# Kernel tuning notes

Hardware: AMD Instinct MI355X
Metric: run time of the kernel (lower is better)

Reference implementation:

```python
import jax, jax.numpy as jnp
import numpy as np

B, S, D = 4, 2048, 1024
E, TOP_K = 8, 2
N_FF = 4096
H = int(2 * N_FF / 3)  # 2730, Expert hidden when ffn_multiplier is None


def setup_inputs() -> dict:
    key = jax.random.key(0)
    ks = jax.random.split(key, 8)
    s = 0.02
    return {
        "x": jax.random.normal(ks[0], (B, S, D), jnp.float32),
        "noise": jax.random.normal(ks[1], (B, S, E), jnp.float32),
        "w_route": jax.random.normal(ks[2], (D, E), jnp.float32) * s,
        "b_route": jnp.zeros((E,), jnp.float32),
        "w_noise": jax.random.normal(ks[3], (D, E), jnp.float32) * s,
        "b_noise": jnp.zeros((E,), jnp.float32),
        "w_proj": jax.random.normal(ks[4], (E, D, 2 * H), jnp.float32) * s,  # SwiGLU proj per expert
        "w_down": jax.random.normal(ks[5], (E, H, D), jnp.float32) * s,
    }


def reference(x, noise, w_route, b_route, w_noise, b_noise, w_proj, w_down):
    b, s, d = x.shape
    e = w_route.shape[1]
    n = b * s
    capacity = int(n * TOP_K / e * 1.0)  # capacity_factor = 1.0

    # --- NoisyTopkRouter (temperature = 1.0) ---
    logits = jnp.einsum("bsd,de->bse", x, w_route) + b_route
    noise_scale = jax.nn.softplus(jnp.einsum("bsd,de->bse", x, w_noise) + b_noise)
    noisy = logits + noise * noise_scale
    top_v, top_i = jax.lax.top_k(noisy, TOP_K)  # [b,s,k]
    # softmax over -inf-filled sparse logits == softmax over the top-k values,
    # scattered back to the expert axis
    probs_k = jax.nn.softmax(top_v, axis=-1)  # [b,s,k]
    routing = jnp.sum(jax.nn.one_hot(top_i, e, dtype=x.dtype) * probs_k[..., None], axis=-2)  # [b,s,e]
    router_prob = routing.mean(axis=(0, 1))
    aux_loss = jnp.sum((router_prob - 1.0 / e) ** 2)

    # --- dispatch ---
    flat_x = x.reshape(n, d)
    flat_gate = routing.reshape(n, e)
    hit = jnp.any(top_i.reshape(n, TOP_K)[:, :, None] == jnp.arange(e)[None, None, :], axis=1)  # [n,e]

    def per_expert(mask_e, gate_e, wp, wd):
        # keep first `capacity` selected tokens, in token order (matches torch nonzero order)
        keep = mask_e & (jnp.cumsum(mask_e) <= capacity)
        sel = jnp.argsort(~keep, stable=True)[:capacity]  # selected token ids first, in order
        valid = keep[sel].astype(flat_x.dtype)
        xin = flat_x[sel]  # [capacity, d]
        x1, x2 = jnp.split(xin @ wp, 2, axis=-1)
        out = (jax.nn.silu(x1) * x2) @ wd  # [capacity, d]
        w = gate_e[sel] * valid
        return sel, out * w[:, None]

    sel, contrib = jax.vmap(per_expert)(hit.T, flat_gate.T, w_proj, w_down)  # [e,cap], [e,cap,d]
    updates = jnp.zeros_like(flat_x).at[sel.reshape(-1)].add(contrib.reshape(-1, d))
    return updates.reshape(b, s, d), aux_loss
```

## Files before the change

kernel.cpp:

```cpp
#include <hip/hip_runtime.h>
#include <cstdint>
#include <cstddef>

#define NTOK 8192
#define DMODEL 1024
#define NEXP 8
#define CAP 2048
#define HFF 2730
#define HFF2 5460
#define KPAD 2752

typedef float f32x4 __attribute__((ext_vector_type(4)));
typedef __attribute__((ext_vector_type(8))) short short8;

__device__ inline unsigned short f2bf(float f) {
  union { float f; unsigned u; } v; v.f = f;
  unsigned u = v.u;
  return (unsigned short)((u + 0x7FFFu + ((u >> 16) & 1u)) >> 16);
}

typedef __attribute__((address_space(1))) const void g_void;
typedef __attribute__((address_space(3))) void l_void;
__device__ __forceinline__ void dma16(const void* g, void* l) {
  __builtin_amdgcn_global_load_lds((g_void*)g, (l_void*)l, 16, 0, 0);
}

__global__ void cast_x_kernel(const float* __restrict__ x, unsigned short* __restrict__ xb) {
  size_t i = ((size_t)blockIdx.x * 256 + threadIdx.x) * 8;
  float4 v0 = *(const float4*)(x + i);
  float4 v1 = *(const float4*)(x + i + 4);
  union { short8 v; unsigned short s[8]; } p;
  p.s[0] = f2bf(v0.x); p.s[1] = f2bf(v0.y); p.s[2] = f2bf(v0.z); p.s[3] = f2bf(v0.w);
  p.s[4] = f2bf(v1.x); p.s[5] = f2bf(v1.y); p.s[6] = f2bf(v1.z); p.s[7] = f2bf(v1.w);
  *(short8*)(xb + i) = p.v;
}

__global__ void router_kernel(const float* __restrict__ x,
                              const float* __restrict__ noise,
                              const float* __restrict__ w_route,
                              const float* __restrict__ b_route,
                              const float* __restrict__ w_noise,
                              const float* __restrict__ b_noise,
                              int* __restrict__ topi,
                              float* __restrict__ gates) {
  const int lane = threadIdx.x & 63;
  const int wave = threadIdx.x >> 6;
  const int tok = blockIdx.x * 4 + wave;
  const float* xr = x + (size_t)tok * DMODEL;

  double aR[8], aN[8];
#pragma unroll
  for (int e = 0; e < 8; e++) { aR[e] = 0.0; aN[e] = 0.0; }

  for (int d = lane; d < DMODEL; d += 64) {
    double xv = (double)xr[d];
    const float* wr = w_route + d * 8;
    const float* wn = w_noise + d * 8;
#pragma unroll
    for (int e = 0; e < 8; e++) {
      aR[e] += xv * (double)wr[e];
      aN[e] += xv * (double)wn[e];
    }
  }
#pragma unroll
  for (int off = 32; off > 0; off >>= 1) {
#pragma unroll
    for (int e = 0; e < 8; e++) {
      aR[e] += __shfl_down(aR[e], (unsigned)off, 64);
      aN[e] += __shfl_down(aN[e], (unsigned)off, 64);
    }
  }
  if (lane == 0) {
    double nv[8];
#pragma unroll
    for (int e = 0; e < 8; e++) {
      double lg = aR[e] + (double)b_route[e];
      double ns = aN[e] + (double)b_noise[e];
      double sp = fmax(ns, 0.0) + log1p(exp(-fabs(ns)));
      nv[e] = lg + (double)noise[(size_t)tok * 8 + e] * sp;
    }
    int i0 = 0;
#pragma unroll
    for (int e = 1; e < 8; e++) if (nv[e] > nv[i0]) i0 = e;
    int i1 = (i0 == 0) ? 1 : 0;
#pragma unroll
    for (int e = 0; e < 8; e++) if (e != i0 && nv[e] > nv[i1]) i1 = e;
    double r = exp(nv[i1] - nv[i0]);
    float g0 = (float)(1.0 / (1.0 + r));
    float g1 = (float)(r / (1.0 + r));
    topi[tok * 2] = i0; topi[tok * 2 + 1] = i1;
    gates[tok * 2] = g0; gates[tok * 2 + 1] = g1;
  }
}

__global__ void aux_kernel(const int* __restrict__ topi,
                           const float* __restrict__ gates,
                           float* __restrict__ out) {
  const int t = threadIdx.x;
  float s[8];
#pragma unroll
  for (int e = 0; e < 8; e++) s[e] = 0.f;
  for (int i = t; i < NTOK; i += 256) {
    int i0 = topi[2 * i], i1 = topi[2 * i + 1];
    float g0 = gates[2 * i], g1 = gates[2 * i + 1];
#pragma unroll
    for (int e = 0; e < 8; e++)
      s[e] += (i0 == e ? g0 : 0.f) + (i1 == e ? g1 : 0.f);
  }
  __shared__ float sh[256][8];
#pragma unroll
  for (int e = 0; e < 8; e++) sh[t][e] = s[e];
  __syncthreads();
  for (int stride = 128; stride > 0; stride >>= 1) {
    if (t < stride) {
#pragma unroll
      for (int e = 0; e < 8; e++) sh[t][e] += sh[t + stride][e];
    }
    __syncthreads();
  }
  if (t == 0) {
    float aux = 0.f;
#pragma unroll
    for (int e = 0; e < 8; e++) {
      float p = sh[0][e] / (float)NTOK - 0.125f;
      aux += p * p;
    }
    out[(size_t)NTOK * DMODEL] = aux;
  }
}

__global__ void dispatch_kernel(const int* __restrict__ topi,
                                const float* __restrict__ gates,
                                int* __restrict__ sel,
                                float* __restrict__ gsel) {
  const int e = blockIdx.x;
  const int t = threadIdx.x;
  const int lane = t & 63;
  const int wave = t >> 6;
  __shared__ int waveSum[4];
  __shared__ int runningS;
  if (t == 0) runningS = 0;
  __syncthreads();

  for (int base = 0; base < NTOK; base += 256) {
    int tok = base + t;
    int i0 = topi[2 * tok], i1 = topi[2 * tok + 1];
    bool hit = (i0 == e) || (i1 == e);
    float g = (i0 == e) ? gates[2 * tok] : gates[2 * tok + 1];
    unsigned long long m = __ballot(hit);
    int prefix = __popcll(m & ((1ull << lane) - 1ull));
    if (lane == 63) waveSum[wave] = prefix + (hit ? 1 : 0);
    __syncthreads();
    int waveOff = 0;
    for (int w = 0; w < wave; w++) waveOff += waveSum[w];
    int pos = runningS + waveOff + prefix;
    if (hit && pos < CAP) { sel[e * CAP + pos] = tok; gsel[e * CAP + pos] = g; }
    __syncthreads();
    if (t == 0) runningS += waveSum[0] + waveSum[1] + waveSum[2] + waveSum[3];
    __syncthreads();
  }
  int total = runningS;
  for (int p = total + t; p < CAP; p += 256) { sel[e * CAP + p] = 0; gsel[e * CAP + p] = 0.f; }
}

__global__ void transpose_wp_kernel(const float* __restrict__ wp,
                                    unsigned short* __restrict__ wpT) {
  const int e = blockIdx.z, d0 = blockIdx.y * 32, f0 = blockIdx.x * 32;
  __shared__ unsigned short tile[32][33];
  const int t = threadIdx.x;
  {
    int ld = t >> 3, lf4 = (t & 7) * 4;
    if (f0 + lf4 < HFF2) {
      float4 v = *(const float4*)(wp + (size_t)e * DMODEL * HFF2 + (size_t)(d0 + ld) * HFF2 + f0 + lf4);
      tile[ld][lf4 + 0] = f2bf(v.x);
      tile[ld][lf4 + 1] = f2bf(v.y);
      tile[ld][lf4 + 2] = f2bf(v.z);
      tile[ld][lf4 + 3] = f2bf(v.w);
    }
  }
  __syncthreads();
  {
    int lf = t >> 3, ldq = (t & 7) * 4;
    if (f0 + lf < HFF2) {
      ushort4 o = make_ushort4(tile[ldq + 0][lf], tile[ldq + 1][lf],
                               tile[ldq + 2][lf], tile[ldq + 3][lf]);
      *(ushort4*)(wpT + (size_t)e * HFF2 * DMODEL + (size_t)(f0 + lf) * DMODEL + d0 + ldq) = o;
    }
  }
}

__global__ void transpose_wd_kernel(const float* __restrict__ wd,
                                    unsigned short* __restrict__ wdT) {
  const int e = blockIdx.z, d0 = blockIdx.y * 32, k0 = blockIdx.x * 32;
  __shared__ unsigned short tile[32][33];
  const int t = threadIdx.x;
  {
    int lk = t >> 3, ld4 = (t & 7) * 4;
    int k = k0 + lk;
    if (k < HFF) {
      float4 v = *(const float4*)(wd + (size_t)e * HFF * DMODEL + (size_t)k * DMODEL + d0 + ld4);
      tile[lk][ld4 + 0] = f2bf(v.x);
      tile[lk][ld4 + 1] = f2bf(v.y);
      tile[lk][ld4 + 2] = f2bf(v.z);
      tile[lk][ld4 + 3] = f2bf(v.w);
    } else {
      tile[lk][ld4 + 0] = 0; tile[lk][ld4 + 1] = 0;
      tile[lk][ld4 + 2] = 0; tile[lk][ld4 + 3] = 0;
    }
  }
  __syncthreads();
  {
    int ld = t >> 3, lkq = (t & 7) * 4;
    ushort4 o = make_ushort4(tile[lkq + 0][ld], tile[lkq + 1][ld],
                             tile[lkq + 2][ld], tile[lkq + 3][ld]);
    *(ushort4*)(wdT + (size_t)e * DMODEL * KPAD + (size_t)(d0 + ld) * KPAD + k0 + lkq) = o;
  }
}

__global__ __launch_bounds__(256, 2)
void gemm1_kernel(const unsigned short* __restrict__ xb,
                  const unsigned short* __restrict__ wpT,
                  const int* __restrict__ sel,
                  unsigned short* __restrict__ h) {
  const int e = blockIdx.z;
  const int m0 = blockIdx.y * 128;
  const int n0 = blockIdx.x * 128;

  __shared__ __align__(16) unsigned short As[128 * 32];
  __shared__ __align__(16) unsigned short B1s[128 * 32];
  __shared__ __align__(16) unsigned short B2s[128 * 32];

  const int t = threadIdx.x;
  const int lane = t & 63;
  const int w = t >> 6;
  const int wm = (w >> 1) * 64;
  const int wn = (w & 1) * 64;
  const int fr = lane & 15;
  const int fq = lane >> 4;

  const int r0 = t >> 2;
  const int seg = (t & 3) * 8;
  const int tok0 = sel[e * CAP + m0 + r0];
  const int tok1 = sel[e * CAP + m0 + 64 + r0];
  const unsigned short* ga0 = xb + (size_t)tok0 * DMODEL + seg;
  const unsigned short* ga1 = xb + (size_t)tok1 * DMODEL + seg;
  const size_t ebase = (size_t)e * HFF2;
  int c0 = n0 + r0;       if (c0 >= HFF) c0 = HFF - 1;
  int c1 = n0 + 64 + r0;  if (c1 >= HFF) c1 = HFF - 1;
  const unsigned short* gb10 = wpT + (ebase + (size_t)c0) * DMODEL + seg;
  const unsigned short* gb11 = wpT + (ebase + (size_t)c1) * DMODEL + seg;
  const unsigned short* gb20 = wpT + (ebase + (size_t)(HFF + c0)) * DMODEL + seg;
  const unsigned short* gb21 = wpT + (ebase + (size_t)(HFF + c1)) * DMODEL + seg;

  unsigned short* aD0 = As + (w * 16) * 32;
  unsigned short* aD1 = As + (64 + w * 16) * 32;
  unsigned short* b1D0 = B1s + (w * 16) * 32;
  unsigned short* b1D1 = B1s + (64 + w * 16) * 32;
  unsigned short* b2D0 = B2s + (w * 16) * 32;
  unsigned short* b2D1 = B2s + (64 + w * 16) * 32;

  f32x4 acc1[4][4], acc2[4][4];
#pragma unroll
  for (int i = 0; i < 4; i++)
#pragma unroll
    for (int j = 0; j < 4; j++) { acc1[i][j] = (f32x4)0.f; acc2[i][j] = (f32x4)0.f; }

  for (int k0 = 0; k0 < DMODEL; k0 += 32) {
    dma16(ga0 + k0, aD0);
    dma16(ga1 + k0, aD1);
    dma16(gb10 + k0, b1D0);
    dma16(gb11 + k0, b1D1);
    dma16(gb20 + k0, b2D0);
    dma16(gb21 + k0, b2D1);
    __syncthreads();

    short8 a[4], b1[4], b2[4];
#pragma unroll
    for (int i = 0; i < 4; i++)
      a[i] = *(const short8*)(As + (wm + i * 16 + fr) * 32 + fq * 8);
#pragma unroll
    for (int j = 0; j < 4; j++) {
      b1[j] = *(const short8*)(B1s + (wn + j * 16 + fr) * 32 + fq * 8);
      b2[j] = *(const short8*)(B2s + (wn + j * 16 + fr) * 32 + fq * 8);
    }
#pragma unroll
    for (int i = 0; i < 4; i++)
#pragma unroll
      for (int j = 0; j < 4; j++) {
        acc1[i][j] = __builtin_amdgcn_mfma_f32_16x16x32_bf16(a[i], b1[j], acc1[i][j], 0, 0, 0);
        acc2[i][j] = __builtin_amdgcn_mfma_f32_16x16x32_bf16(a[i], b2[j], acc2[i][j], 0, 0, 0);
      }
    __syncthreads();
  }

#pragma unroll
  for (int i = 0; i < 4; i++) {
#pragma unroll
    for (int j = 0; j < 4; j++) {
      const int col = n0 + wn + j * 16 + fr;
      if (col < KPAD) {
#pragma unroll
        for (int r = 0; r < 4; r++) {
          const int row = m0 + wm + i * 16 + fq * 4 + r;
          float v1 = acc1[i][j][r], v2 = acc2[i][j][r];
          float hv = (col < HFF) ? (v1 / (1.f + __expf(-v1))) * v2 : 0.f;
          h[((size_t)e * CAP + row) * KPAD + col] = f2bf(hv);
        }
      }
    }
  }
}

__global__ __launch_bounds__(256, 2)
void gemm2_kernel(const unsigned short* __restrict__ h,
                  const unsigned short* __restrict__ wdT,
                  const int* __restrict__ sel,
                  const float* __restrict__ gsel,
                  float* __restrict__ out) {
  const int e = blockIdx.z;
  const int m0 = blockIdx.y * 128;
  const int n0 = blockIdx.x * 128;

  __shared__ __align__(16) unsigned short As[128 * 32];
  __shared__ __align__(16) unsigned short Bs[128 * 32];
  __shared__ int selS[128];
  __shared__ float gS[128];

  const int t = threadIdx.x;
  if (t < 128) { selS[t] = sel[e * CAP + m0 + t]; gS[t] = gsel[e * CAP + m0 + t]; }

  const int lane = t & 63;
  const int w = t >> 6;
  const int wm = (w >> 1) * 64;
  const int wn = (w & 1) * 64;
  const int fr = lane & 15;
  const int fq = lane >> 4;

  const int r0 = t >> 2;
  const int seg = (t & 3) * 8;
  const unsigned short* ga0 = h + ((size_t)e * CAP + m0 + r0) * KPAD + seg;
  const unsigned short* ga1 = h + ((size_t)e * CAP + m0 + 64 + r0) * KPAD + seg;
  const unsigned short* gb0 = wdT + ((size_t)e * DMODEL + n0 + r0) * KPAD + seg;
  const unsigned short* gb1 = wdT + ((size_t)e * DMODEL + n0 + 64 + r0) * KPAD + seg;

  unsigned short* aD0 = As + (w * 16) * 32;
  unsigned short* aD1 = As + (64 + w * 16) * 32;
  unsigned short* bD0 = Bs + (w * 16) * 32;
  unsigned short* bD1 = Bs + (64 + w * 16) * 32;

  f32x4 acc[4][4];
#pragma unroll
  for (int i = 0; i < 4; i++)
#pragma unroll
    for (int j = 0; j < 4; j++) acc[i][j] = (f32x4)0.f;

  for (int k0 = 0; k0 < KPAD; k0 += 32) {
    dma16(ga0 + k0, aD0);
    dma16(ga1 + k0, aD1);
    dma16(gb0 + k0, bD0);
    dma16(gb1 + k0, bD1);
    __syncthreads();

    short8 a[4], b[4];
#pragma unroll
    for (int i = 0; i < 4; i++)
      a[i] = *(const short8*)(As + (wm + i * 16 + fr) * 32 + fq * 8);
#pragma unroll
    for (int j = 0; j < 4; j++)
      b[j] = *(const short8*)(Bs + (wn + j * 16 + fr) * 32 + fq * 8);
#pragma unroll
    for (int i = 0; i < 4; i++)
#pragma unroll
      for (int j = 0; j < 4; j++)
        acc[i][j] = __builtin_amdgcn_mfma_f32_16x16x32_bf16(a[i], b[j], acc[i][j], 0, 0, 0);
    __syncthreads();
  }

#pragma unroll
  for (int i = 0; i < 4; i++) {
#pragma unroll
    for (int j = 0; j < 4; j++) {
      const int col = n0 + wn + j * 16 + fr;
#pragma unroll
      for (int r = 0; r < 4; r++) {
        const int rowL = wm + i * 16 + fq * 4 + r;
        float g = gS[rowL];
        if (g != 0.f) {
          int token = selS[rowL];
          atomicAdd(&out[(size_t)token * DMODEL + col], acc[i][j][r] * g);
        }
      }
    }
  }
}

extern "C" void kernel_launch(void* const* d_in, const int* in_sizes, int n_in,
                              void* d_out, int out_size, void* d_ws, size_t ws_size,
                              hipStream_t stream) {
  const float* x = (const float*)d_in[0];
  const float* noise = (const float*)d_in[1];
  const float* w_route = (const float*)d_in[2];
  const float* b_route = (const float*)d_in[3];
  const float* w_noise = (const float*)d_in[4];
  const float* b_noise = (const float*)d_in[5];
  const float* w_proj = (const float*)d_in[6];
  const float* w_down = (const float*)d_in[7];
  float* out = (float*)d_out;

  char* ws = (char*)d_ws;
  const size_t WT_BYTES = (size_t)NEXP * HFF2 * DMODEL * 2;
  const size_t H_BYTES = (size_t)NEXP * CAP * KPAD * 2;
  unsigned short* wT = (unsigned short*)ws;
  unsigned short* hbuf = (unsigned short*)(ws + WT_BYTES);
  char* p = ws + WT_BYTES + H_BYTES;
  int* sel = (int*)p;          p += (size_t)NEXP * CAP * 4;
  float* gsel = (float*)p;     p += (size_t)NEXP * CAP * 4;
  int* topi = (int*)p;         p += (size_t)NTOK * 2 * 4;
  float* gates = (float*)p;

  unsigned short* xb = (unsigned short*)d_out;

  hipLaunchKernelGGL(cast_x_kernel, dim3(NTOK * DMODEL / (256 * 8)), dim3(256), 0, stream, x, xb);
  hipLaunchKernelGGL(router_kernel, dim3(NTOK / 4), dim3(256), 0, stream,
                     x, noise, w_route, b_route, w_noise, b_noise, topi, gates);
  hipLaunchKernelGGL(dispatch_kernel, dim3(NEXP), dim3(256), 0, stream, topi, gates, sel, gsel);
  hipLaunchKernelGGL(transpose_wp_kernel, dim3(171, 32, NEXP), dim3(256), 0, stream, w_proj, wT);
  hipLaunchKernelGGL(gemm1_kernel, dim3(22, 16, NEXP), dim3(256), 0, stream, xb, wT, sel, hbuf);

  hipMemsetAsync(d_out, 0, (size_t)out_size * sizeof(float), stream);
  hipLaunchKernelGGL(aux_kernel, dim3(1), dim3(256), 0, stream, topi, gates, out);
  hipLaunchKernelGGL(transpose_wd_kernel, dim3(KPAD / 32, DMODEL / 32, NEXP), dim3(256), 0, stream, w_down, wT);
  hipLaunchKernelGGL(gemm2_kernel, dim3(DMODEL / 128, CAP / 128, NEXP), dim3(256), 0, stream,
                     hbuf, wT, sel, gsel, out);
}
```

Measured before the change: 927.1 us.

## Double-buffer swizzled GEMM tiles and replace atomic scatter with gather combine

Result: faster. 850.2 us (-8.3%).

```diff
diff --git a/kernel.cpp b/kernel.cpp
--- a/kernel.cpp
+++ b/kernel.cpp
@@ -17,6 +17,9 @@
   union { float f; unsigned u; } v; v.f = f;
   unsigned u = v.u;
   return (unsigned short)((u + 0x7FFFu + ((u >> 16) & 1u)) >> 16);
+}
+__device__ inline float bf2f(unsigned short s) {
+  union { unsigned u; float f; } v; v.u = ((unsigned)s) << 16; return v.f;
 }
 
 typedef __attribute__((address_space(1))) const void g_void;
@@ -132,35 +135,48 @@
 __global__ void dispatch_kernel(const int* __restrict__ topi,
                                 const float* __restrict__ gates,
                                 int* __restrict__ sel,
-                                float* __restrict__ gsel) {
+                                float* __restrict__ gsel,
+                                int* __restrict__ slot) {
   const int e = blockIdx.x;
   const int t = threadIdx.x;
   const int lane = t & 63;
-  const int wave = t >> 6;
-  __shared__ int waveSum[4];
+  const int w = t >> 6;
+  __shared__ int waveCnt[16];
   __shared__ int runningS;
   if (t == 0) runningS = 0;
   __syncthreads();
 
-  for (int base = 0; base < NTOK; base += 256) {
+  for (int base = 0; base < NTOK; base += 1024) {
     int tok = base + t;
     int i0 = topi[2 * tok], i1 = topi[2 * tok + 1];
     bool hit = (i0 == e) || (i1 == e);
-    float g = (i0 == e) ? gates[2 * tok] : gates[2 * tok + 1];
+    int kth = (i0 == e) ? 0 : 1;
+    float g = gates[2 * tok + kth];
     unsigned long long m = __ballot(hit);
     int prefix = __popcll(m & ((1ull << lane) - 1ull));
-    if (lane == 63) waveSum[wave] = prefix + (hit ? 1 : 0);
-    __syncthreads();
-    int waveOff = 0;
-    for (int w = 0; w < wave; w++) waveOff += waveSum[w];
-    int pos = runningS + waveOff + prefix;
-    if (hit && pos < CAP) { sel[e * CAP + pos] = tok; gsel[e * CAP + pos] = g; }
-    __syncthreads();
-    if (t == 0) runningS += waveSum[0] + waveSum[1] + waveSum[2] + waveSum[3];
-    __syncthreads();
-  }
-  int total = runningS;
-  for (int p = total + t; p < CAP; p += 256) { sel[e * CAP + p] = 0; gsel[e * CAP + p] = 0.f; }
+    if (lane == 63) waveCnt[w] = prefix + (hit ? 1 : 0);
+    __syncthreads();
+    int off = runningS;
+    for (int ww = 0; ww < w; ww++) off += waveCnt[ww];
+    int pos = off + prefix;
+    if (hit) {
+      if (pos < CAP) {
+        sel[e * CAP + pos] = tok; gsel[e * CAP + pos] = g;
+        slot[2 * tok + kth] = pos;
+      } else {
+        slot[2 * tok + kth] = -1;
+      }
+    }
+    __syncthreads();
+    if (t == 0) {
+      int sacc = 0;
+#pragma unroll
+      for (int ww = 0; ww < 16; ww++) sacc += waveCnt[ww];
+      runningS += sacc;
+    }
+    __syncthreads();
+  }
+  for (int p = runningS + t; p < CAP; p += 1024) { sel[e * CAP + p] = 0; gsel[e * CAP + p] = 0.f; }
 }
 
 __global__ void transpose_wp_kernel(const float* __restrict__ wp,
@@ -223,12 +239,12 @@
                   const int* __restrict__ sel,
                   unsigned short* __restrict__ h) {
   const int e = blockIdx.z;
-  const int m0 = blockIdx.y * 128;
-  const int n0 = blockIdx.x * 128;
-
-  __shared__ __align__(16) unsigned short As[128 * 32];
-  __shared__ __align__(16) unsigned short B1s[128 * 32];
-  __shared__ __align__(16) unsigned short B2s[128 * 32];
+  const int m0 = blockIdx.x * 128;
+  const int n0 = blockIdx.y * 128;
+
+  __shared__ __align__(16) unsigned short As[2 * 4096];
+  __shared__ __align__(16) unsigned short B1s[2 * 4096];
+  __shared__ __align__(16) unsigned short B2s[2 * 4096];
 
   const int t = threadIdx.x;
   const int lane = t & 63;
@@ -237,27 +253,23 @@
   const int wn = (w & 1) * 64;
   const int fr = lane & 15;
   const int fq = lane >> 4;
+  const int csw = (fq ^ ((fr >> 1) & 3)) * 8;
 
   const int r0 = t >> 2;
-  const int seg = (t & 3) * 8;
+  const int sw = ((t & 3) ^ ((t >> 3) & 3)) * 8;
   const int tok0 = sel[e * CAP + m0 + r0];
   const int tok1 = sel[e * CAP + m0 + 64 + r0];
-  const unsigned short* ga0 = xb + (size_t)tok0 * DMODEL + seg;
-  const unsigned short* ga1 = xb + (size_t)tok1 * DMODEL + seg;
+  const unsigned short* ga0 = xb + (size_t)tok0 * DMODEL + sw;
+  const unsigned short* ga1 = xb + (size_t)tok1 * DMODEL + sw;
   const size_t ebase = (size_t)e * HFF2;
   int c0 = n0 + r0;       if (c0 >= HFF) c0 = HFF - 1;
   int c1 = n0 + 64 + r0;  if (c1 >= HFF) c1 = HFF - 1;
-  const unsigned short* gb10 = wpT + (ebase + (size_t)c0) * DMODEL + seg;
-  const unsigned short* gb11 = wpT + (ebase + (size_t)c1) * DMODEL + seg;
-  const unsigned short* gb20 = wpT + (ebase + (size_t)(HFF + c0)) * DMODEL + seg;
-  const unsigned short* gb21 = wpT + (ebase + (size_t)(HFF + c1)) * DMODEL + seg;
-
-  unsigned short* aD0 = As + (w * 16) * 32;
-  unsigned short* aD1 = As + (64 + w * 16) * 32;
-  unsigned short* b1D0 = B1s + (w * 16) * 32;
-  unsigned short* b1D1 = B1s + (64 + w * 16) * 32;
-  unsigned short* b2D0 = B2s + (w * 16) * 32;
-  unsigned short* b2D1 = B2s + (64 + w * 16) * 32;
+  const unsigned short* gb10 = wpT + (ebase + (size_t)c0) * DMODEL + sw;
+  const unsigned short* gb11 = wpT + (ebase + (size_t)c1) * DMODEL + sw;
+  const unsigned short* gb20 = wpT + (ebase + (size_t)(HFF + c0)) * DMODEL + sw;
+  const unsigned short* gb21 = wpT + (ebase + (size_t)(HFF + c1)) * DMODEL + sw;
+
+  const int dOff = (w * 16) * 32;
 
   f32x4 acc1[4][4], acc2[4][4];
 #pragma unroll
@@ -265,23 +277,33 @@
 #pragma unroll
     for (int j = 0; j < 4; j++) { acc1[i][j] = (f32x4)0.f; acc2[i][j] = (f32x4)0.f; }
 
+  auto stage = [&](int k0, int buf) {
+    const int bo = buf * 4096;
+    dma16(ga0 + k0, As + bo + dOff);
+    dma16(ga1 + k0, As + bo + 2048 + dOff);
+    dma16(gb10 + k0, B1s + bo + dOff);
+    dma16(gb11 + k0, B1s + bo + 2048 + dOff);
+    dma16(gb20 + k0, B2s + bo + dOff);
+    dma16(gb21 + k0, B2s + bo + 2048 + dOff);
+  };
+
+  stage(0, 0);
   for (int k0 = 0; k0 < DMODEL; k0 += 32) {
-    dma16(ga0 + k0, aD0);
-    dma16(ga1 + k0, aD1);
-    dma16(gb10 + k0, b1D0);
-    dma16(gb11 + k0, b1D1);
-    dma16(gb20 + k0, b2D0);
-    dma16(gb21 + k0, b2D1);
-    __syncthreads();
-
+    const int cur = (k0 >> 5) & 1;
+    __syncthreads();
+    if (k0 + 32 < DMODEL) stage(k0 + 32, cur ^ 1);
+
+    const unsigned short* Ab = As + cur * 4096;
+    const unsigned short* B1b = B1s + cur * 4096;
+    const unsigned short* B2b = B2s + cur * 4096;
     short8 a[4], b1[4], b2[4];
 #pragma unroll
     for (int i = 0; i < 4; i++)
-      a[i] = *(const short8*)(As + (wm + i * 16 + fr) * 32 + fq * 8);
+      a[i] = *(const short8*)(Ab + (wm + i * 16 + fr) * 32 + csw);
 #pragma unroll
     for (int j = 0; j < 4; j++) {
-      b1[j] = *(const short8*)(B1s + (wn + j * 16 + fr) * 32 + fq * 8);
-      b2[j] = *(const short8*)(B2s + (wn + j * 16 + fr) * 32 + fq * 8);
+      b1[j] = *(const short8*)(B1b + (wn + j * 16 + fr) * 32 + csw);
+      b2[j] = *(const short8*)(B2b + (wn + j * 16 + fr) * 32 + csw);
     }
 #pragma unroll
     for (int i = 0; i < 4; i++)
@@ -290,7 +312,6 @@
         acc1[i][j] = __builtin_amdgcn_mfma_f32_16x16x32_bf16(a[i], b1[j], acc1[i][j], 0, 0, 0);
         acc2[i][j] = __builtin_amdgcn_mfma_f32_16x16x32_bf16(a[i], b2[j], acc2[i][j], 0, 0, 0);
       }
-    __syncthreads();
   }
 
 #pragma unroll
@@ -311,42 +332,34 @@
   }
 }
 
-__global__ __launch_bounds__(256, 2)
+__global__ __launch_bounds__(256, 3)
 void gemm2_kernel(const unsigned short* __restrict__ h,
                   const unsigned short* __restrict__ wdT,
-                  const int* __restrict__ sel,
-                  const float* __restrict__ gsel,
-                  float* __restrict__ out) {
+                  unsigned short* __restrict__ contrib) {
   const int e = blockIdx.z;
-  const int m0 = blockIdx.y * 128;
-  const int n0 = blockIdx.x * 128;
-
-  __shared__ __align__(16) unsigned short As[128 * 32];
-  __shared__ __align__(16) unsigned short Bs[128 * 32];
-  __shared__ int selS[128];
-  __shared__ float gS[128];
-
-  const int t = threadIdx.x;
-  if (t < 128) { selS[t] = sel[e * CAP + m0 + t]; gS[t] = gsel[e * CAP + m0 + t]; }
-
+  const int m0 = blockIdx.x * 128;
+  const int n0 = blockIdx.y * 128;
+
+  __shared__ __align__(16) unsigned short As[2 * 4096];
+  __shared__ __align__(16) unsigned short Bs[2 * 4096];
+
+  const int t = threadIdx.x;
   const int lane = t & 63;
   const int w = t >> 6;
   const int wm = (w >> 1) * 64;
   const int wn = (w & 1) * 64;
   const int fr = lane & 15;
   const int fq = lane >> 4;
+  const int csw = (fq ^ ((fr >> 1) & 3)) * 8;
 
   const int r0 = t >> 2;
-  const int seg = (t & 3) * 8;
-  const unsigned short* ga0 = h + ((size_t)e * CAP + m0 + r0) * KPAD + seg;
-  const unsigned short* ga1 = h + ((size_t)e * CAP + m0 + 64 + r0) * KPAD + seg;
-  const unsigned short* gb0 = wdT + ((size_t)e * DMODEL + n0 + r0) * KPAD + seg;
-  const unsigned short* gb1 = wdT + ((size_t)e * DMODEL + n0 + 64 + r0) * KPAD + seg;
-
-  unsigned short* aD0 = As + (w * 16) * 32;
-  unsigned short* aD1 = As + (64 + w * 16) * 32;
-  unsigned short* bD0 = Bs + (w * 16) * 32;
-  unsigned short* bD1 = Bs + (64 + w * 16) * 32;
+  const int sw = ((t & 3) ^ ((t >> 3) & 3)) * 8;
+  const unsigned short* ga0 = h + ((size_t)e * CAP + m0 + r0) * KPAD + sw;
+  const unsigned short* ga1 = h + ((size_t)e * CAP + m0 + 64 + r0) * KPAD + sw;
+  const unsigned short* gb0 = wdT + ((size_t)e * DMODEL + n0 + r0) * KPAD + sw;
+  const unsigned short* gb1 = wdT + ((size_t)e * DMODEL + n0 + 64 + r0) * KPAD + sw;
+
+  const int dOff = (w * 16) * 32;
 
   f32x4 acc[4][4];
 #pragma unroll
@@ -354,26 +367,34 @@
 #pragma unroll
     for (int j = 0; j < 4; j++) acc[i][j] = (f32x4)0.f;
 
+  auto stage = [&](int k0, int buf) {
+    const int bo = buf * 4096;
+    dma16(ga0 + k0, As + bo + dOff);
+    dma16(ga1 + k0, As + bo + 2048 + dOff);
+    dma16(gb0 + k0, Bs + bo + dOff);
+    dma16(gb1 + k0, Bs + bo + 2048 + dOff);
+  };
+
+  stage(0, 0);
   for (int k0 = 0; k0 < KPAD; k0 += 32) {
-    dma16(ga0 + k0, aD0);
-    dma16(ga1 + k0, aD1);
-    dma16(gb0 + k0, bD0);
-    dma16(gb1 + k0, bD1);
-    __syncthreads();
-
+    const int cur = (k0 >> 5) & 1;
+    __syncthreads();
+    if (k0 + 32 < KPAD) stage(k0 + 32, cur ^ 1);
+
+    const unsigned short* Ab = As + cur * 4096;
+    const unsigned short* Bb = Bs + cur * 4096;
     short8 a[4], b[4];
 #pragma unroll
     for (int i = 0; i < 4; i++)
-      a[i] = *(const short8*)(As + (wm + i * 16 + fr) * 32 + fq * 8);
+      a[i] = *(const short8*)(Ab + (wm + i * 16 + fr) * 32 + csw);
 #pragma unroll
     for (int j = 0; j < 4; j++)
-      b[j] = *(const short8*)(Bs + (wn + j * 16 + fr) * 32 + fq * 8);
+      b[j] = *(const short8*)(Bb + (wn + j * 16 + fr) * 32 + csw);
 #pragma unroll
     for (int i = 0; i < 4; i++)
 #pragma unroll
       for (int j = 0; j < 4; j++)
         acc[i][j] = __builtin_amdgcn_mfma_f32_16x16x32_bf16(a[i], b[j], acc[i][j], 0, 0, 0);
-    __syncthreads();
   }
 
 #pragma unroll
@@ -383,15 +404,35 @@
       const int col = n0 + wn + j * 16 + fr;
 #pragma unroll
       for (int r = 0; r < 4; r++) {
-        const int rowL = wm + i * 16 + fq * 4 + r;
-        float g = gS[rowL];
-        if (g != 0.f) {
-          int token = selS[rowL];
-          atomicAdd(&out[(size_t)token * DMODEL + col], acc[i][j][r] * g);
-        }
+        const int row = m0 + wm + i * 16 + fq * 4 + r;
+        contrib[((size_t)e * CAP + row) * DMODEL + col] = f2bf(acc[i][j][r]);
       }
     }
   }
+}
+
+__global__ void combine_kernel(const unsigned short* __restrict__ contrib,
+                               const int* __restrict__ topi,
+                               const int* __restrict__ slot,
+                               const float* __restrict__ gates,
+                               float* __restrict__ out) {
+  const int tok = blockIdx.x;
+  const int t = threadIdx.x;
+  const int e0 = topi[2 * tok], e1 = topi[2 * tok + 1];
+  const int s0 = slot[2 * tok], s1 = slot[2 * tok + 1];
+  const float g0 = gates[2 * tok], g1 = gates[2 * tok + 1];
+  float4 acc = make_float4(0.f, 0.f, 0.f, 0.f);
+  if (s0 >= 0) {
+    ushort4 c = *(const ushort4*)(contrib + ((size_t)(e0 * CAP + s0)) * DMODEL + t * 4);
+    acc.x += g0 * bf2f(c.x); acc.y += g0 * bf2f(c.y);
+    acc.z += g0 * bf2f(c.z); acc.w += g0 * bf2f(c.w);
+  }
+  if (s1 >= 0) {
+    ushort4 c = *(const ushort4*)(contrib + ((size_t)(e1 * CAP + s1)) * DMODEL + t * 4);
+    acc.x += g1 * bf2f(c.x); acc.y += g1 * bf2f(c.y);
+    acc.z += g1 * bf2f(c.z); acc.w += g1 * bf2f(c.w);
+  }
+  *(float4*)(out + (size_t)tok * DMODEL + t * 4) = acc;
 }
 
 extern "C" void kernel_launch(void* const* d_in, const int* in_sizes, int n_in,
@@ -409,27 +450,30 @@
 
   char* ws = (char*)d_ws;
   const size_t WT_BYTES = (size_t)NEXP * HFF2 * DMODEL * 2;
+  const size_t WDT_BYTES = (size_t)NEXP * DMODEL * KPAD * 2;
   const size_t H_BYTES = (size_t)NEXP * CAP * KPAD * 2;
   unsigned short* wT = (unsigned short*)ws;
+  unsigned short* contrib = (unsigned short*)(ws + WDT_BYTES);
   unsigned short* hbuf = (unsigned short*)(ws + WT_BYTES);
   char* p = ws + WT_BYTES + H_BYTES;
   int* sel = (int*)p;          p += (size_t)NEXP * CAP * 4;
   float* gsel = (float*)p;     p += (size_t)NEXP * CAP * 4;
   int* topi = (int*)p;         p += (size_t)NTOK * 2 * 4;
-  float* gates = (float*)p;
+  float* gates = (float*)p;    p += (size_t)NTOK * 2 * 4;
+  int* slot = (int*)p;
 
   unsigned short* xb = (unsigned short*)d_out;
 
   hipLaunchKernelGGL(cast_x_kernel, dim3(NTOK * DMODEL / (256 * 8)), dim3(256), 0, stream, x, xb);
   hipLaunchKernelGGL(router_kernel, dim3(NTOK / 4), dim3(256), 0, stream,
                      x, noise, w_route, b_route, w_noise, b_noise, topi, gates);
-  hipLaunchKernelGGL(dispatch_kernel, dim3(NEXP), dim3(256), 0, stream, topi, gates, sel, gsel);
+  hipLaunchKernelGGL(dispatch_kernel, dim3(NEXP), dim3(1024), 0, stream, topi, gates, sel, gsel, slot);
   hipLaunchKernelGGL(transpose_wp_kernel, dim3(171, 32, NEXP), dim3(256), 0, stream, w_proj, wT);
-  hipLaunchKernelGGL(gemm1_kernel, dim3(22, 16, NEXP), dim3(256), 0, stream, xb, wT, sel, hbuf);
-
-  hipMemsetAsync(d_out, 0, (size_t)out_size * sizeof(float), stream);
+  hipLaunchKernelGGL(gemm1_kernel, dim3(16, 22, NEXP), dim3(256), 0, stream, xb, wT, sel, hbuf);
+  hipLaunchKernelGGL(transpose_wd_kernel, dim3(KPAD / 32, DMODEL / 32, NEXP), dim3(256), 0, stream, w_down, wT);
+  hipLaunchKernelGGL(gemm2_kernel, dim3(16, DMODEL / 128, NEXP), dim3(256), 0, stream,
+                     hbuf, wT, contrib);
+  hipLaunchKernelGGL(combine_kernel, dim3(NTOK), dim3(256), 0, stream,
+                     contrib, topi, slot, gates, out);
   hipLaunchKernelGGL(aux_kernel, dim3(1), dim3(256), 0, stream, topi, gates, out);
-  hipLaunchKernelGGL(transpose_wd_kernel, dim3(KPAD / 32, DMODEL / 32, NEXP), dim3(256), 0, stream, w_down, wT);
-  hipLaunchKernelGGL(gemm2_kernel, dim3(DMODEL / 128, CAP / 128, NEXP), dim3(256), 0, stream,
-                     hbuf, wT, sel, gsel, out);
-}
+}
```
